# Performance work log

Measured on AMD Instinct MI355X. Metric: run time of the kernel, lower is better.

## Reference

```python
import jax, jax.numpy as jnp
import numpy as np

B, N, D = 4, 4096, 1024
HEADS, DIM_HEAD = 16, 64
INNER = HEADS * DIM_HEAD
LN_EPS = 1e-5


def next_fast_len(n):
    # smallest 5-smooth integer >= n (matches scipy.fftpack.next_fast_len)
    while True:
        m = n
        for p in (2, 3, 5):
            while m % p == 0:
                m //= p
        if m == 1:
            return n
        n += 1


def setup_inputs() -> dict:
    key = jax.random.key(0)
    k = jax.random.split(key, 6)
    x = jax.random.normal(k[0], (B, N, D), dtype=jnp.float32)
    gamma = jnp.ones((D,), dtype=jnp.float32)
    beta = jnp.zeros((D,), dtype=jnp.float32)
    alpha = jax.random.normal(k[1], (HEADS,), dtype=jnp.float32)
    w_in = jax.random.normal(k[2], (INNER, D), dtype=jnp.float32) * 0.02
    w_out = jax.random.normal(k[3], (D, INNER), dtype=jnp.float32) * 0.02
    return {"x": x, "gamma": gamma, "beta": beta, "alpha": alpha, "w_in": w_in, "w_out": w_out}


def reference(x, gamma, beta, alpha, w_in, w_out):
    b, n, d = x.shape
    h, dh = HEADS, DIM_HEAD
    # LayerNorm (biased variance, eps=1e-5)
    mu = jnp.mean(x, axis=-1, keepdims=True)
    var = jnp.var(x, axis=-1, keepdims=True)
    xn = (x - mu) * jax.lax.rsqrt(var + LN_EPS) * gamma + beta
    # project_in (no bias), split heads: b n (h d) -> b h n d
    xi = jnp.einsum('bnd,ed->bne', xn, w_in)
    xi = xi.reshape(b, n, h, dh).transpose(0, 2, 1, 3)  # [b,h,n,dh]
    # exponential decay weights per head: alpha * (1-alpha)**flip(arange(n)) -> [h, n]
    a = jax.nn.sigmoid(alpha)[:, None]
    weights = a * (1.0 - a) ** jnp.arange(n - 1, -1, -1, dtype=x.dtype)[None, :]
    # FFT-based causal correlation (conv1d_fft)
    fast_len = next_fast_len(n + n - 1)
    f_x = jnp.fft.rfft(xi, n=fast_len, axis=-2)           # [b,h,L',dh] complex
    f_w = jnp.fft.rfft(weights, n=fast_len, axis=-1)      # [h,L'] complex
    out = jnp.fft.irfft(f_x * jnp.conj(f_w)[None, :, :, None], fast_len, axis=-2)
    out = jnp.roll(out, -1, axis=-2)
    out = out[:, :, fast_len - n:, :]                      # last n positions -> [b,h,n,dh]
    # merge heads and project out
    out = out.transpose(0, 2, 1, 3).reshape(b, n, h * dh)
    return jnp.einsum('bne,de->bnd', out, w_out)
```

## Files before the change

### kernel.cpp

```cpp
#include <hip/hip_runtime.h>
#include <hip/hip_bf16.h>

#define B_ 4
#define N_ 4096
#define D_ 1024
#define H_ 16
#define INNER_ 1024
#define M_ (B_ * N_)
#define CH_ 128
#define CL_ 32

using bf16x8 = __attribute__((ext_vector_type(8))) __bf16;
using f32x4  = __attribute__((ext_vector_type(4))) float;

__device__ __forceinline__ float bf2f(unsigned short v) {
  return __uint_as_float(((unsigned)v) << 16);
}
__device__ __forceinline__ unsigned short f2bf(float f) {
  __hip_bfloat16 h = __float2bfloat16(f);
  return *reinterpret_cast<unsigned short*>(&h);
}
__device__ __forceinline__ float sigm(float x) { return 1.f / (1.f + expf(-x)); }

__device__ __forceinline__ void gload_lds16(const void* g, void* l) {
  __builtin_amdgcn_global_load_lds(
      (const __attribute__((address_space(1))) unsigned int*)g,
      (__attribute__((address_space(3))) unsigned int*)l, 16, 0, 0);
}

#define W4_ ((INNER_ * D_) / 4)
__global__ __launch_bounds__(256) void lncast_kernel(
    const float* __restrict__ x, const float* __restrict__ gamma,
    const float* __restrict__ beta, __hip_bfloat16* __restrict__ xn,
    const float* __restrict__ wa, const float* __restrict__ wb,
    __hip_bfloat16* __restrict__ oa, __hip_bfloat16* __restrict__ ob) {
  if (blockIdx.x < 2048) {
    int i = blockIdx.x * 256 + threadIdx.x;
    const float* src = (i < W4_) ? wa : wb;
    __hip_bfloat16* dst = (i < W4_) ? oa : ob;
    int j = (i < W4_) ? i : i - W4_;
    float4 v = reinterpret_cast<const float4*>(src)[j];
    ushort4 o;
    o.x = f2bf(v.x); o.y = f2bf(v.y); o.z = f2bf(v.z); o.w = f2bf(v.w);
    reinterpret_cast<ushort4*>(dst)[j] = o;
    return;
  }
  const long row = blockIdx.x - 2048;
  const int t = threadIdx.x;
  const float4 v = reinterpret_cast<const float4*>(x + row * D_)[t];
  float s = v.x + v.y + v.z + v.w;
  float s2 = v.x * v.x + v.y * v.y + v.z * v.z + v.w * v.w;
#pragma unroll
  for (int o = 32; o > 0; o >>= 1) {
    s += __shfl_down(s, o);
    s2 += __shfl_down(s2, o);
  }
  __shared__ float red[8];
  const int lane = t & 63, wv = t >> 6;
  if (lane == 0) { red[wv] = s; red[4 + wv] = s2; }
  __syncthreads();
  const float sum = red[0] + red[1] + red[2] + red[3];
  const float sum2 = red[4] + red[5] + red[6] + red[7];
  const float mu = sum * (1.f / D_);
  const float var = sum2 * (1.f / D_) - mu * mu;
  const float rs = rsqrtf(var + 1e-5f);
  const float4 g = reinterpret_cast<const float4*>(gamma)[t];
  const float4 bb = reinterpret_cast<const float4*>(beta)[t];
  ushort4 o;
  o.x = f2bf((v.x - mu) * rs * g.x + bb.x);
  o.y = f2bf((v.y - mu) * rs * g.y + bb.y);
  o.z = f2bf((v.z - mu) * rs * g.z + bb.z);
  o.w = f2bf((v.w - mu) * rs * g.w + bb.w);
  reinterpret_cast<ushort4*>(xn + row * D_)[t] = o;
}

__device__ __forceinline__ void stc(float* p, float v) { *p = v; }
__device__ __forceinline__ void stc(__hip_bfloat16* p, float v) { *p = __float2bfloat16(v); }

template <typename TOUT, int NT, bool FUSE>
__global__ __launch_bounds__(512, 2) void gemm256_kernel(
    const __hip_bfloat16* __restrict__ A, const __hip_bfloat16* __restrict__ Bt,
    TOUT* __restrict__ C, float* __restrict__ finals, const float* __restrict__ alpha,
    int M, int N, int K) {
  static_assert(NT >= 4, "ring needs >=4 tiles");
  __shared__ __align__(16) char lds[131072];
  const int tid = threadIdx.x;
  const int lane = tid & 63;
  const int wave = tid >> 6;

  int wg = blockIdx.y * gridDim.x + blockIdx.x;
  wg = (wg & 7) * 32 + (wg >> 3);
  const int bx = wg & 3;
  const int by = wg >> 2;
  const long bm = (long)by * 256;
  const long bn = (long)bx * 256;

  const int u0  = (tid & 7) ^ ((tid >> 3) & 7);
  const int r0  = 2 * (tid >> 3) + (u0 >> 2);
  const int ck0 = u0 & 3;
  const __hip_bfloat16* sA0 = A  + (bm + r0) * (long)K + ck0 * 8;
  const __hip_bfloat16* sA1 = sA0 + 128l * K;
  const __hip_bfloat16* sB0 = Bt + (bn + r0) * (long)K + ck0 * 8;
  const __hip_bfloat16* sB1 = sB0 + 128l * K;
  char* dbase = (char*)lds + wave * 1024;

  const int wm = wave >> 2;
  const int wn = wave & 3;
  const int fr = lane & 15;
  const int ck = lane >> 4;
  const int pos = (((fr & 1) << 2) | ck) ^ ((fr >> 1) & 7);
  const int laneA = wm * 8192 + (fr >> 1) * 128 + pos * 16;
  const int laneB = 16384 + wn * 4096 + (fr >> 1) * 128 + pos * 16;

  f32x4 acc[8][4] = {};

#define STAGE_A(kt) do { const int _s = (kt) & 3;                         \
    gload_lds16(sA0 + (long)(kt) * 32, dbase + _s * 32768);               \
    gload_lds16(sA1 + (long)(kt) * 32, dbase + _s * 32768 + 8192); } while (0)
#define STAGE_B(kt) do { const int _s = (kt) & 3;                         \
    gload_lds16(sB0 + (long)(kt) * 32, dbase + _s * 32768 + 16384);       \
    gload_lds16(sB1 + (long)(kt) * 32, dbase + _s * 32768 + 24576); } while (0)

  STAGE_A(0); STAGE_B(0);
  STAGE_A(1); STAGE_B(1);
  asm volatile("s_waitcnt vmcnt(4)" ::: "memory");
  __builtin_amdgcn_s_barrier();
  asm volatile("" ::: "memory");

#pragma unroll 4
  for (int t = 0; t < NT; ++t) {
    const char* base = (const char*)lds + (t & 3) * 32768;
    bf16x8 bv[4], av[4];
#pragma unroll
    for (int c = 0; c < 4; ++c) bv[c] = *(const bf16x8*)(base + laneB + c * 1024);
#pragma unroll
    for (int r = 0; r < 4; ++r) av[r] = *(const bf16x8*)(base + laneA + r * 1024);
    if (t + 2 < NT) STAGE_A(t + 2);
    __builtin_amdgcn_s_setprio(1);
#pragma unroll
    for (int r = 0; r < 4; ++r)
#pragma unroll
      for (int c = 0; c < 4; ++c)
        acc[r][c] = __builtin_amdgcn_mfma_f32_16x16x32_bf16(av[r], bv[c], acc[r][c], 0, 0, 0);
    __builtin_amdgcn_s_setprio(0);
#pragma unroll
    for (int r = 0; r < 4; ++r) av[r] = *(const bf16x8*)(base + laneA + (r + 4) * 1024);
    if (t + 2 < NT) STAGE_B(t + 2);
    __builtin_amdgcn_s_setprio(1);
#pragma unroll
    for (int r = 0; r < 4; ++r)
#pragma unroll
      for (int c = 0; c < 4; ++c)
        acc[r + 4][c] = __builtin_amdgcn_mfma_f32_16x16x32_bf16(av[r], bv[c], acc[r + 4][c], 0, 0, 0);
    __builtin_amdgcn_s_setprio(0);
    if (t < NT - 3) asm volatile("s_waitcnt vmcnt(4)" ::: "memory");
    else            asm volatile("s_waitcnt vmcnt(0)" ::: "memory");
    __builtin_amdgcn_s_barrier();
    asm volatile("" ::: "memory");
  }
#undef STAGE_A
#undef STAGE_B

  const int cr = ck * 4;
#pragma unroll
  for (int rf = 0; rf < 8; ++rf)
#pragma unroll
    for (int cf = 0; cf < 4; ++cf)
#pragma unroll
      for (int r = 0; r < 4; ++r) {
        const long row = bm + wm * 128 + rf * 16 + cr + r;
        const long col = bn + wn * 64 + cf * 16 + fr;
        stc(&C[row * (long)N + col], acc[rf][cf][r]);
      }

  if constexpr (FUSE) {
    const int head = (int)((bn + wn * 64) >> 6);
    const float a = sigm(alpha[head]);
    const float lw = log2f(1.f - a);
    float wgt[2][4];
#pragma unroll
    for (int p = 0; p < 2; ++p)
#pragma unroll
      for (int r = 0; r < 4; ++r)
        wgt[p][r] = exp2f((float)(31 - (p * 16 + cr + r)) * lw);
#pragma unroll
    for (int q = 0; q < 4; ++q) {
#pragma unroll
      for (int cf = 0; cf < 4; ++cf) {
        float s = 0.f;
#pragma unroll
        for (int p = 0; p < 2; ++p)
#pragma unroll
          for (int r = 0; r < 4; ++r)
            s += wgt[p][r] * acc[q * 2 + p][cf][r];
        s += __shfl_xor(s, 16);
        s += __shfl_xor(s, 32);
        if (ck == 0) {
          const long row0 = bm + wm * 128 + q * 32;
          const long bb = row0 >> 12;
          const long cq = (row0 >> 5) & 127;
          const int e = (int)bn + wn * 64 + cf * 16 + fr;
          finals[(bb * CH_ + cq) * INNER_ + e] = a * s;
        }
      }
    }
  }
}

__global__ __launch_bounds__(256) void scan_carry_kernel(
    const float* __restrict__ finals, float* __restrict__ carries,
    const float* __restrict__ alpha) {
  const int g = blockIdx.x * 256 + threadIdx.x;
  const int b = g >> 10;
  const int e = g & 1023;
  const float a = sigm(alpha[e >> 6]);
  const float dc = powf(1.f - a, (float)CL_);
  float carry = 0.f;
  for (int c = 0; c < CH_; ++c) {
    const long idx = ((long)b * CH_ + c) * INNER_ + e;
    carries[idx] = carry;
    carry = finals[idx] + dc * carry;
  }
}

__global__ __launch_bounds__(256) void scan_apply_kernel(
    const __hip_bfloat16* __restrict__ xi, __hip_bfloat16* __restrict__ y,
    const float* __restrict__ carries, const float* __restrict__ alpha) {
  const int e0 = threadIdx.x * 4;
  const int c = blockIdx.y;
  const int b = blockIdx.z;
  const float a = sigm(alpha[e0 >> 6]);
  const float om = 1.f - a;
  const float4 cr = *reinterpret_cast<const float4*>(
      &carries[((long)b * CH_ + c) * INNER_ + e0]);
  float y0 = cr.x, y1 = cr.y, y2 = cr.z, y3 = cr.w;
  long base = ((long)b * N_ + (long)c * CL_) * INNER_ + e0;
  for (int t = 0; t < CL_; ++t) {
    ushort4 u = *(const ushort4*)(xi + base);
    y0 = om * y0 + a * bf2f(u.x);
    y1 = om * y1 + a * bf2f(u.y);
    y2 = om * y2 + a * bf2f(u.z);
    y3 = om * y3 + a * bf2f(u.w);
    ushort4 o;
    o.x = f2bf(y0); o.y = f2bf(y1); o.z = f2bf(y2); o.w = f2bf(y3);
    *(ushort4*)(y + base) = o;
    base += INNER_;
  }
}

extern "C" void kernel_launch(void* const* d_in, const int* in_sizes, int n_in,
                              void* d_out, int out_size, void* d_ws, size_t ws_size,
                              hipStream_t stream) {
  const float* x     = (const float*)d_in[0];
  const float* gamma = (const float*)d_in[1];
  const float* beta  = (const float*)d_in[2];
  const float* alpha = (const float*)d_in[3];
  const float* w_in  = (const float*)d_in[4];
  const float* w_out = (const float*)d_in[5];
  float* out = (float*)d_out;
  char* ws = (char*)d_ws;

  __hip_bfloat16* xn = (__hip_bfloat16*)ws;
  __hip_bfloat16* wi = (__hip_bfloat16*)(ws + (32l << 20));
  __hip_bfloat16* wo = (__hip_bfloat16*)(ws + (34l << 20));
  float* finals      = (float*)(ws + (36l << 20));
  float* carries     = (float*)(ws + (38l << 20));
  __hip_bfloat16* xi = (__hip_bfloat16*)d_out;

  lncast_kernel<<<2048 + M_, 256, 0, stream>>>(x, gamma, beta, xn, w_in, w_out, wi, wo);

  gemm256_kernel<__hip_bfloat16, 32, true>
      <<<dim3(INNER_ / 256, M_ / 256), 512, 0, stream>>>(xn, wi, xi, finals, alpha,
                                                         M_, INNER_, D_);

  __hip_bfloat16* y = xn;
  scan_carry_kernel<<<(B_ * INNER_) / 256, 256, 0, stream>>>(finals, carries, alpha);
  scan_apply_kernel<<<dim3(1, CH_, B_), 256, 0, stream>>>(xi, y, carries, alpha);

  gemm256_kernel<float, 32, false>
      <<<dim3(D_ / 256, M_ / 256), 512, 0, stream>>>(y, wo, out, nullptr, nullptr,
                                                     M_, D_, INNER_);
}
```

Before: 123.4 us.

## Shrink GEMM tiles to 128x256 with a three-slot LDS ring

Both GEMMs now use 128x256 output tiles instead of 256x256. Each wave holds a 4x4 accumulator block, and the launch grid doubles in the M dimension. The LDS ring goes from four 32KB slots to three 24KB slots using pointer rotation, cutting LDS to 72KB and accumulator registers so that more workgroups can be resident per CU. The trade-off is lower arithmetic intensity per tile, with more redundant B-matrix loads. The tile-swizzle constant and the fused decay-sum epilogue are adjusted to match the new tile size.

```diff
diff --git a/kernel.cpp b/kernel.cpp
--- a/kernel.cpp
+++ b/kernel.cpp
@@ -78,99 +78,95 @@
 __device__ __forceinline__ void stc(__hip_bfloat16* p, float v) { *p = __float2bfloat16(v); }
 
 template <typename TOUT, int NT, bool FUSE>
-__global__ __launch_bounds__(512, 2) void gemm256_kernel(
+__global__ __launch_bounds__(512, 4) void gemm128_kernel(
     const __hip_bfloat16* __restrict__ A, const __hip_bfloat16* __restrict__ Bt,
     TOUT* __restrict__ C, float* __restrict__ finals, const float* __restrict__ alpha,
     int M, int N, int K) {
   static_assert(NT >= 4, "ring needs >=4 tiles");
-  __shared__ __align__(16) char lds[131072];
+  __shared__ __align__(16) char lds[73728];
   const int tid = threadIdx.x;
   const int lane = tid & 63;
   const int wave = tid >> 6;
 
   int wg = blockIdx.y * gridDim.x + blockIdx.x;
-  wg = (wg & 7) * 32 + (wg >> 3);
+  wg = (wg & 7) * 64 + (wg >> 3);
   const int bx = wg & 3;
   const int by = wg >> 2;
-  const long bm = (long)by * 256;
+  const long bm = (long)by * 128;
   const long bn = (long)bx * 256;
 
   const int u0  = (tid & 7) ^ ((tid >> 3) & 7);
   const int r0  = 2 * (tid >> 3) + (u0 >> 2);
   const int ck0 = u0 & 3;
-  const __hip_bfloat16* sA0 = A  + (bm + r0) * (long)K + ck0 * 8;
-  const __hip_bfloat16* sA1 = sA0 + 128l * K;
+  const __hip_bfloat16* sA  = A  + (bm + r0) * (long)K + ck0 * 8;
   const __hip_bfloat16* sB0 = Bt + (bn + r0) * (long)K + ck0 * 8;
   const __hip_bfloat16* sB1 = sB0 + 128l * K;
-  char* dbase = (char*)lds + wave * 1024;
+  const int wb16 = wave * 1024;
 
   const int wm = wave >> 2;
   const int wn = wave & 3;
   const int fr = lane & 15;
   const int ck = lane >> 4;
   const int pos = (((fr & 1) << 2) | ck) ^ ((fr >> 1) & 7);
-  const int laneA = wm * 8192 + (fr >> 1) * 128 + pos * 16;
-  const int laneB = 16384 + wn * 4096 + (fr >> 1) * 128 + pos * 16;
-
-  f32x4 acc[8][4] = {};
-
-#define STAGE_A(kt) do { const int _s = (kt) & 3;                         \
-    gload_lds16(sA0 + (long)(kt) * 32, dbase + _s * 32768);               \
-    gload_lds16(sA1 + (long)(kt) * 32, dbase + _s * 32768 + 8192); } while (0)
-#define STAGE_B(kt) do { const int _s = (kt) & 3;                         \
-    gload_lds16(sB0 + (long)(kt) * 32, dbase + _s * 32768 + 16384);       \
-    gload_lds16(sB1 + (long)(kt) * 32, dbase + _s * 32768 + 24576); } while (0)
-
-  STAGE_A(0); STAGE_B(0);
-  STAGE_A(1); STAGE_B(1);
-  asm volatile("s_waitcnt vmcnt(4)" ::: "memory");
+  const int rbase = (fr >> 1) * 128 + pos * 16;
+  const int laneA = wm * 4096 + rbase;
+  const int laneB = 8192 + wn * 4096 + rbase;
+
+  f32x4 acc[4][4] = {};
+
+  char* slot0 = (char*)lds;
+  char* slot1 = (char*)lds + 24576;
+  char* slot2 = (char*)lds + 49152;
+
+#define STAGE(sl, kt) do {                                                \
+    gload_lds16(sA  + (long)(kt) * 32, (sl) + wb16);                      \
+    gload_lds16(sB0 + (long)(kt) * 32, (sl) + 8192 + wb16);               \
+    gload_lds16(sB1 + (long)(kt) * 32, (sl) + 16384 + wb16); } while (0)
+
+  STAGE(slot0, 0);
+  STAGE(slot1, 1);
+  asm volatile("s_waitcnt vmcnt(3)" ::: "memory");
   __builtin_amdgcn_s_barrier();
   asm volatile("" ::: "memory");
 
+  char* cur = slot0;
+  char* nxt = slot1;
+  char* stg = slot2;
 #pragma unroll 4
   for (int t = 0; t < NT; ++t) {
-    const char* base = (const char*)lds + (t & 3) * 32768;
-    bf16x8 bv[4], av[4];
-#pragma unroll
-    for (int c = 0; c < 4; ++c) bv[c] = *(const bf16x8*)(base + laneB + c * 1024);
-#pragma unroll
-    for (int r = 0; r < 4; ++r) av[r] = *(const bf16x8*)(base + laneA + r * 1024);
-    if (t + 2 < NT) STAGE_A(t + 2);
+    bf16x8 av[4], bv[4];
+#pragma unroll
+    for (int j = 0; j < 4; ++j) bv[j] = *(const bf16x8*)(cur + laneB + j * 1024);
+#pragma unroll
+    for (int i = 0; i < 4; ++i) av[i] = *(const bf16x8*)(cur + laneA + i * 1024);
+    if (t + 2 < NT) STAGE(stg, t + 2);
     __builtin_amdgcn_s_setprio(1);
 #pragma unroll
-    for (int r = 0; r < 4; ++r)
-#pragma unroll
-      for (int c = 0; c < 4; ++c)
-        acc[r][c] = __builtin_amdgcn_mfma_f32_16x16x32_bf16(av[r], bv[c], acc[r][c], 0, 0, 0);
+    for (int i = 0; i < 4; ++i)
+#pragma unroll
+      for (int j = 0; j < 4; ++j)
+        acc[i][j] = __builtin_amdgcn_mfma_f32_16x16x32_bf16(av[i], bv[j], acc[i][j], 0, 0, 0);
     __builtin_amdgcn_s_setprio(0);
-#pragma unroll
-    for (int r = 0; r < 4; ++r) av[r] = *(const bf16x8*)(base + laneA + (r + 4) * 1024);
-    if (t + 2 < NT) STAGE_B(t + 2);
-    __builtin_amdgcn_s_setprio(1);
-#pragma unroll
-    for (int r = 0; r < 4; ++r)
-#pragma unroll
-      for (int c = 0; c < 4; ++c)
-        acc[r + 4][c] = __builtin_amdgcn_mfma_f32_16x16x32_bf16(av[r], bv[c], acc[r + 4][c], 0, 0, 0);
-    __builtin_amdgcn_s_setprio(0);
-    if (t < NT - 3) asm volatile("s_waitcnt vmcnt(4)" ::: "memory");
-    else            asm volatile("s_waitcnt vmcnt(0)" ::: "memory");
-    __builtin_amdgcn_s_barrier();
-    asm volatile("" ::: "memory");
-  }
-#undef STAGE_A
-#undef STAGE_B
+    if (t + 2 < NT)      asm volatile("s_waitcnt vmcnt(3)" ::: "memory");
+    else if (t + 1 < NT) asm volatile("s_waitcnt vmcnt(0)" ::: "memory");
+    if (t + 1 < NT) {
+      __builtin_amdgcn_s_barrier();
+      asm volatile("" ::: "memory");
+    }
+    char* tmp = cur; cur = nxt; nxt = stg; stg = tmp;
+  }
+#undef STAGE
 
   const int cr = ck * 4;
 #pragma unroll
-  for (int rf = 0; rf < 8; ++rf)
-#pragma unroll
-    for (int cf = 0; cf < 4; ++cf)
+  for (int i = 0; i < 4; ++i)
+#pragma unroll
+    for (int j = 0; j < 4; ++j)
 #pragma unroll
       for (int r = 0; r < 4; ++r) {
-        const long row = bm + wm * 128 + rf * 16 + cr + r;
-        const long col = bn + wn * 64 + cf * 16 + fr;
-        stc(&C[row * (long)N + col], acc[rf][cf][r]);
+        const long row = bm + wm * 64 + i * 16 + cr + r;
+        const long col = bn + wn * 64 + j * 16 + fr;
+        stc(&C[row * (long)N + col], acc[i][j][r]);
       }
 
   if constexpr (FUSE) {
@@ -184,7 +180,7 @@
       for (int r = 0; r < 4; ++r)
         wgt[p][r] = exp2f((float)(31 - (p * 16 + cr + r)) * lw);
 #pragma unroll
-    for (int q = 0; q < 4; ++q) {
+    for (int q = 0; q < 2; ++q) {
 #pragma unroll
       for (int cf = 0; cf < 4; ++cf) {
         float s = 0.f;
@@ -196,7 +192,7 @@
         s += __shfl_xor(s, 16);
         s += __shfl_xor(s, 32);
         if (ck == 0) {
-          const long row0 = bm + wm * 128 + q * 32;
+          const long row0 = bm + wm * 64 + q * 32;
           const long bb = row0 >> 12;
           const long cq = (row0 >> 5) & 127;
           const int e = (int)bn + wn * 64 + cf * 16 + fr;
@@ -269,15 +265,15 @@
 
   lncast_kernel<<<2048 + M_, 256, 0, stream>>>(x, gamma, beta, xn, w_in, w_out, wi, wo);
 
-  gemm256_kernel<__hip_bfloat16, 32, true>
-      <<<dim3(INNER_ / 256, M_ / 256), 512, 0, stream>>>(xn, wi, xi, finals, alpha,
+  gemm128_kernel<__hip_bfloat16, 32, true>
+      <<<dim3(INNER_ / 256, M_ / 128), 512, 0, stream>>>(xn, wi, xi, finals, alpha,
                                                          M_, INNER_, D_);
 
   __hip_bfloat16* y = xn;
   scan_carry_kernel<<<(B_ * INNER_) / 256, 256, 0, stream>>>(finals, carries, alpha);
   scan_apply_kernel<<<dim3(1, CH_, B_), 256, 0, stream>>>(xi, y, carries, alpha);
 
-  gemm256_kernel<float, 32, false>
-      <<<dim3(D_ / 256, M_ / 256), 512, 0, stream>>>(y, wo, out, nullptr, nullptr,
+  gemm128_kernel<float, 32, false>
+      <<<dim3(D_ / 256, M_ / 128), 512, 0, stream>>>(y, wo, out, nullptr, nullptr,
                                                      M_, D_, INNER_);
 }
```

After: 188.5 us. 1.53x slower.
